# Performance work log

Hardware: AMD Instinct MI355X
Metric: run time of the kernel (lower is better)

The kernel has to match this reference:

```python
import jax, jax.numpy as jnp
import numpy as np

# geomloss SamplesLoss('sinkhorn', p=2, debias=True, reach=0.3, blur=0.01) constants
P = 2
BLUR = 0.01
REACH = 0.3
RHO = REACH ** P            # unbalanced KL strength rho = reach^p = 0.09
SCALING = 0.5               # geomloss default epsilon-scaling factor
DIAMETER = 1.0              # static diameter estimate (jit-friendly schedule)


def _eps_list():
    # geomloss epsilon_schedule(p, diameter, blur, scaling)
    eps = [DIAMETER ** P]
    eps += list(np.exp(np.arange(P * np.log(DIAMETER), P * np.log(BLUR), P * np.log(SCALING))))
    eps.append(BLUR ** P)
    return [float(e) for e in eps]


def _cost(x, y):
    # geomloss p=2 cost: |x - y|^2 / 2, shape [N, M]
    x2 = jnp.sum(x * x, axis=-1)[:, None]
    y2 = jnp.sum(y * y, axis=-1)[None, :]
    return 0.5 * (x2 + y2 - 2.0 * jnp.matmul(x, y.T))


def _softmin(eps, C, h):
    # h: log-weights (+ potential/eps), shape [M]; returns shape [N]
    return -eps * jax.nn.logsumexp(h[None, :] - C / eps, axis=1)


def _sinkhorn_divergence(x, y):
    N, M = x.shape[0], y.shape[0]
    a_log = jnp.full((N,), -np.log(N), dtype=x.dtype)   # uniform weights
    b_log = jnp.full((M,), -np.log(M), dtype=y.dtype)

    C_xy = _cost(x, y)
    C_yx = C_xy.T
    C_xx = _cost(x, x)
    C_yy = _cost(y, y)

    sg = jax.lax.stop_gradient
    Cxy_d, Cyx_d, Cxx_d, Cyy_d = sg(C_xy), sg(C_yx), sg(C_xx), sg(C_yy)

    eps_list = _eps_list()
    damp = lambda eps: 1.0 / (1.0 + eps / RHO)  # unbalanced dampening

    # init at largest blur (geomloss sinkhorn_loop)
    eps0 = eps_list[0]
    d0 = damp(eps0)
    g_ab = d0 * _softmin(eps0, Cyx_d, a_log)
    f_ba = d0 * _softmin(eps0, Cxy_d, b_log)
    f_aa = d0 * _softmin(eps0, Cxx_d, a_log)
    g_bb = d0 * _softmin(eps0, Cyy_d, b_log)

    # symmetric Sinkhorn updates with epsilon annealing (no grad, as in geomloss)
    for eps in eps_list:
        d = damp(eps)
        ft_ba = d * _softmin(eps, Cxy_d, b_log + g_ab / eps)
        gt_ab = d * _softmin(eps, Cyx_d, a_log + f_ba / eps)
        f_ba, g_ab = 0.5 * (f_ba + ft_ba), 0.5 * (g_ab + gt_ab)
        ft_aa = d * _softmin(eps, Cxx_d, a_log + f_aa / eps)
        gt_bb = d * _softmin(eps, Cyy_d, b_log + g_bb / eps)
        f_aa, g_bb = 0.5 * (f_aa + ft_aa), 0.5 * (g_bb + gt_bb)

    # last extrapolation at final blur, differentiable w.r.t. the cost
    eps = eps_list[-1]
    d = damp(eps)
    f_ba, g_ab = (d * _softmin(eps, C_xy, b_log + sg(g_ab) / eps),
                  d * _softmin(eps, C_yx, a_log + sg(f_ba) / eps))
    f_aa = d * _softmin(eps, C_xx, a_log + sg(f_aa) / eps)
    g_bb = d * _softmin(eps, C_yy, b_log + sg(g_bb) / eps)

    # unbalanced debiased Sinkhorn cost (geomloss sinkhorn_cost + UnbalancedWeight)
    a = jnp.exp(a_log)
    b = jnp.exp(b_log)
    w = RHO + eps / 2.0
    loss = w * (jnp.dot(a, jnp.exp(-f_aa / RHO) - jnp.exp(-f_ba / RHO))
                + jnp.dot(b, jnp.exp(-g_bb / RHO) - jnp.exp(-g_ab / RHO)))
    return loss


def setup_inputs() -> dict:
    key = jax.random.key(0)
    k1, k2, k3 = jax.random.split(key, 3)
    B, H, W = 512, 128, 128
    unnormed = jax.random.uniform(k1, (B, 1, H, W), dtype=jnp.float32)
    nd = jax.random.uniform(k2, (B, 1, H, W), dtype=jnp.float32)
    gt = jax.random.uniform(k3, (B, 1, H, W), dtype=jnp.float32)
    # normalized density maps sum to 1 per sample (as in DM-Count)
    nd = nd / jnp.sum(nd, axis=(1, 2, 3), keepdims=True)
    gt = gt / jnp.sum(gt, axis=(1, 2, 3), keepdims=True)
    return {"unnormed_density": unnormed, "normed_density": nd, "gt": gt}


def reference(unnormed_density, normed_density, gt):
    x = normed_density.reshape(normed_density.shape[0], -1)  # [B, HW]
    y = gt.reshape(gt.shape[0], -1)                          # [B, HW]
    loss = _sinkhorn_divergence(x, y)
    wd = 0
    ot_obj_values = jnp.zeros((1,), dtype=jnp.float32)
    return (loss, wd, ot_obj_values)
```

## Files before the change

### kernel.cpp

```cpp
#include <hip/hip_runtime.h>
#include <math.h>

#define HW 16384
#define NPTS 1024
#define LOG_N 6.2383246250395075
#define RHO_C 0.09
#define SCALE_F 16384.0f
#define INV_SCALE2 3.725290298461914e-09
#define NTILES 36

typedef _Float16 f16x8 __attribute__((ext_vector_type(8)));
typedef float f32x4 __attribute__((ext_vector_type(4)));

typedef __attribute__((address_space(1))) const void gvoid_t;
typedef __attribute__((address_space(3))) void svoid_t;

__device__ __forceinline__ void tri_map(int tt, int& ti, int& tj) {
  int a = 0, r = tt;
  while (r >= 8 - a) { r -= 8 - a; ++a; }
  ti = a; tj = a + r;
}

__global__ __launch_bounds__(256)
void convert_split_k(const float* __restrict__ nd, const float* __restrict__ gt,
                     _Float16* __restrict__ hi_t, _Float16* __restrict__ lo_t) {
  const int wt = blockIdx.x * 4 + (threadIdx.x >> 6);
  const int lane = threadIdx.x & 63;
  const int k64 = wt >> 6;
  const int rb = (wt & 63) << 4;
  const int g = lane & 7;
#pragma unroll
  for (int p = 0; p < 2; ++p) {
    const int row = rb + p * 8 + (lane >> 3);
    const float* __restrict__ src =
        (row < 512 ? nd + (size_t)row * HW : gt + (size_t)(row - 512) * HW) +
        k64 * 64 + g * 8;
    const float4 v0 = *(const float4*)(src);
    const float4 v1 = *(const float4*)(src + 4);
    const float x[8] = {v0.x, v0.y, v0.z, v0.w, v1.x, v1.y, v1.z, v1.w};
    f16x8 h, l;
#pragma unroll
    for (int j = 0; j < 8; ++j) {
      const float xs = x[j] * SCALE_F;
      const _Float16 hh = (_Float16)xs;
      h[j] = hh;
      l[j] = (_Float16)(xs - (float)hh);
    }
    const size_t o = ((size_t)k64 * 1024 + row) * 64 + (size_t)((g ^ (row & 7)) * 8);
    *(f16x8*)(hi_t + o) = h;
    *(f16x8*)(lo_t + o) = l;
  }
}

__global__ __launch_bounds__(512, 2)
void gemm_mfma_k(const _Float16* __restrict__ hi_t, const _Float16* __restrict__ lo_t,
                 float* __restrict__ part, int ns) {
  extern __shared__ _Float16 lds[];

  const int nwg = NTILES * ns;
  const int b = blockIdx.x;
  const int k8 = b & 7, i8 = b >> 3;
  const int q8 = nwg >> 3, r8 = nwg & 7;
  const int start = (k8 < r8) ? k8 * (q8 + 1) : r8 * (q8 + 1) + (k8 - r8) * q8;
  const int lin = start + i8;
  const int c = lin / NTILES, tt = lin - c * NTILES;

  int ti, tj;
  tri_map(tt, ti, tj);
  const bool dtile = (ti == tj);
  const int q = 256 / ns, rm = 256 - q * ns;
  const int kt0 = c * q + (c < rm ? c : rm);
  const int nkt = q + (c < rm ? 1 : 0);
  const int t = threadIdx.x;
  const int lane = t & 63, w = t >> 6;
  const int pr = (w >> 1) & 1, pc = w & 1;
  const int h = w >> 2;
  const int rlow = lane & 15, g0 = lane >> 4;
  const int sw = rlow & 7;
  const int boff = dtile ? 0 : 16384;

  f32x4 acc[4][4];
#pragma unroll
  for (int m = 0; m < 4; ++m)
#pragma unroll
    for (int n = 0; n < 4; ++n) acc[m][n] = (f32x4){0.f, 0.f, 0.f, 0.f};

#define STAGE(BUF, KT)                                                          \
  {                                                                             \
    const size_t tb_ = (size_t)(KT) * 65536;                                    \
    const size_t ga_ = tb_ + (size_t)ti * 8192 + w * 1024 + lane * 8;           \
    _Float16* lb_ = lds + (BUF) * 32768 + w * 1024;                             \
    __builtin_amdgcn_global_load_lds((gvoid_t*)(hi_t + ga_), (svoid_t*)(lb_), 16, 0, 0);               \
    __builtin_amdgcn_global_load_lds((gvoid_t*)(hi_t + ga_ + 512), (svoid_t*)(lb_ + 512), 16, 0, 0);   \
    __builtin_amdgcn_global_load_lds((gvoid_t*)(lo_t + ga_), (svoid_t*)(lb_ + 8192), 16, 0, 0);        \
    __builtin_amdgcn_global_load_lds((gvoid_t*)(lo_t + ga_ + 512), (svoid_t*)(lb_ + 8704), 16, 0, 0);  \
    if (!dtile) {                                                               \
      const size_t gb_ = tb_ + (size_t)tj * 8192 + w * 1024 + lane * 8;         \
      __builtin_amdgcn_global_load_lds((gvoid_t*)(hi_t + gb_), (svoid_t*)(lb_ + 16384), 16, 0, 0);     \
      __builtin_amdgcn_global_load_lds((gvoid_t*)(hi_t + gb_ + 512), (svoid_t*)(lb_ + 16896), 16, 0, 0);\
      __builtin_amdgcn_global_load_lds((gvoid_t*)(lo_t + gb_), (svoid_t*)(lb_ + 24576), 16, 0, 0);     \
      __builtin_amdgcn_global_load_lds((gvoid_t*)(lo_t + gb_ + 512), (svoid_t*)(lb_ + 25088), 16, 0, 0);\
    }                                                                           \
  }

  STAGE(0, kt0);
  __syncthreads();

  int cur = 0;
  for (int ks = 0; ks < nkt; ++ks) {
    if (ks + 1 < nkt) STAGE(cur ^ 1, kt0 + ks + 1);
    __builtin_amdgcn_sched_barrier(0);

    const _Float16* __restrict__ bb = lds + cur * 32768;
    const int pe = ((h * 4 + g0) ^ sw) * 8;
    f16x8 ah[4], al[4], bh[4], bl[4];
#pragma unroll
    for (int m = 0; m < 4; ++m) {
      const int ra = pr * 64 + m * 16 + rlow;
      ah[m] = *(const f16x8*)(bb + ra * 64 + pe);
      al[m] = *(const f16x8*)(bb + 8192 + ra * 64 + pe);
      const int rb = pc * 64 + m * 16 + rlow;
      bh[m] = *(const f16x8*)(bb + boff + rb * 64 + pe);
      bl[m] = *(const f16x8*)(bb + boff + 8192 + rb * 64 + pe);
    }

    __builtin_amdgcn_s_setprio(1);
#pragma unroll
    for (int m = 0; m < 4; ++m)
#pragma unroll
      for (int n = 0; n < 4; ++n) {
        acc[m][n] = __builtin_amdgcn_mfma_f32_16x16x32_f16(ah[m], bh[n], acc[m][n], 0, 0, 0);
        acc[m][n] = __builtin_amdgcn_mfma_f32_16x16x32_f16(al[m], bh[n], acc[m][n], 0, 0, 0);
        acc[m][n] = __builtin_amdgcn_mfma_f32_16x16x32_f16(ah[m], bl[n], acc[m][n], 0, 0, 0);
      }
    __builtin_amdgcn_s_setprio(0);
    __syncthreads();
    cur ^= 1;
  }

  float* red = (float*)lds;
  if (h == 1) {
    float* wb = red + (w & 3) * 4096;
#pragma unroll
    for (int m = 0; m < 4; ++m)
#pragma unroll
      for (int n = 0; n < 4; ++n)
        *(f32x4*)(wb + (m * 4 + n) * 256 + lane * 4) = acc[m][n];
  }
  __syncthreads();
  if (h == 0) {
    float* wb = red + w * 4096;
    float* __restrict__ dst = part + ((size_t)c * NTILES + tt) * 16384;
    const int clb = pc * 64 + rlow;
    const int rlb = pr * 64 + g0 * 4;
#pragma unroll
    for (int m = 0; m < 4; ++m)
#pragma unroll
      for (int n = 0; n < 4; ++n) {
        const f32x4 o = *(const f32x4*)(wb + (m * 4 + n) * 256 + lane * 4);
        const f32x4 s = acc[m][n] + o;
#pragma unroll
        for (int p = 0; p < 4; ++p)
          dst[(rlb + m * 16 + p) * 128 + clb + n * 16] = s[p];
      }
  }
#undef STAGE
}

__global__ __launch_bounds__(256)
void reduce_tiles_k(const float* __restrict__ part, float* __restrict__ G,
                    float* __restrict__ diag, int nsplit) {
  __shared__ float sl[8][129];
  const int blk = blockIdx.x;
  const int tt = blk >> 4, s = blk & 15;
  int ti, tj;
  tri_map(tt, ti, tj);
  const int t = threadIdx.x;
  const int base_in = tt * 16384 + s * 1024;

  float vals[4];
#pragma unroll
  for (int j = 0; j < 4; ++j) {
    const int idx = j * 256 + t;
    double a = 0.0;
    for (int c = 0; c < nsplit; ++c)
      a += (double)part[(size_t)c * (NTILES * 16384) + base_in + idx];
    vals[j] = (float)(a * INV_SCALE2);
  }
#pragma unroll
  for (int j = 0; j < 4; ++j) {
    const int idx = j * 256 + t;
    const int r = idx >> 7, cl = idx & 127;
    const int R = ti * 128 + s * 8 + r, C = tj * 128 + cl;
    G[(size_t)R * NPTS + C] = vals[j];
    if (R == C) diag[R] = vals[j];
    sl[r][cl] = vals[j];
  }
  if (ti == tj) return;
  __syncthreads();
#pragma unroll
  for (int j = 0; j < 4; ++j) {
    const int idx = j * 256 + t;
    const int r = idx & 7, cl = idx >> 3;
    G[(size_t)(tj * 128 + cl) * NPTS + ti * 128 + s * 8 + r] = sl[r][cl];
  }
}

__global__ __launch_bounds__(256)
void sinkhorn_phase_k(const float* __restrict__ G, const float* __restrict__ diag,
                      const double* __restrict__ src, double* __restrict__ dst,
                      double eps, double inv_eps, double damp, int use_pot,
                      int do_avg) {
  const int w = threadIdx.x >> 6, lane = threadIdx.x & 63;
  const int id = blockIdx.x * 4 + w;
  const int which = id >> 9, r = id & 511;
  int row_pt, col_base, pot_idx;
  if (which == 0)      { row_pt = r;       col_base = 512; pot_idx = 1; }
  else if (which == 1) { row_pt = 512 + r; col_base = 0;   pot_idx = 0; }
  else if (which == 2) { row_pt = r;       col_base = 0;   pot_idx = 2; }
  else                 { row_pt = 512 + r; col_base = 512; pot_idx = 3; }

  const double dr = (double)diag[row_pt];
  const double* __restrict__ pot = src + pot_idx * 512;
  const float* __restrict__ Grow = G + (size_t)row_pt * NPTS + col_base;
  const float* __restrict__ dcol = diag + col_base;

  double arg[8];
  double m = -1.0e300;
#pragma unroll
  for (int u = 0; u < 8; ++u) {
    const int j = lane + u * 64;
    const double C = 0.5 * (dr + (double)dcol[j]) - (double)Grow[j];
    const double p = use_pot ? pot[j] : 0.0;
    const double a = (p - C) * inv_eps - LOG_N;
    arg[u] = a;
    m = fmax(m, a);
  }
#pragma unroll
  for (int off = 32; off > 0; off >>= 1) m = fmax(m, __shfl_xor(m, off));
  double s = 0.0;
#pragma unroll
  for (int u = 0; u < 8; ++u) s += exp(arg[u] - m);
#pragma unroll
  for (int off = 32; off > 0; off >>= 1) s += __shfl_xor(s, off);
  if (lane == 0) {
    const double lse = m + log(s);
    const double val = -eps * lse * damp;
    dst[which * 512 + r] = do_avg ? 0.5 * (src[which * 512 + r] + val) : val;
  }
}

__global__ __launch_bounds__(256)
void loss_k(const double* __restrict__ pot, float* __restrict__ out, int out_size,
            double w) {
  const int t = threadIdx.x;
  double s = 0.0;
  for (int i = t; i < 512; i += 256) {
    s += (exp(-pot[1024 + i] / RHO_C) - exp(-pot[i] / RHO_C)) +
         (exp(-pot[1536 + i] / RHO_C) - exp(-pot[512 + i] / RHO_C));
  }
#pragma unroll
  for (int off = 32; off > 0; off >>= 1) s += __shfl_xor(s, off);
  __shared__ double wsum[4];
  if ((t & 63) == 0) wsum[t >> 6] = s;
  __syncthreads();
  if (t == 0) {
    out[0] = (float)(w * (wsum[0] + wsum[1] + wsum[2] + wsum[3]) * (1.0 / 512.0));
    for (int i = 1; i < out_size; ++i) out[i] = 0.f;
  }
}

extern "C" void kernel_launch(void* const* d_in, const int* in_sizes, int n_in,
                              void* d_out, int out_size, void* d_ws, size_t ws_size,
                              hipStream_t stream) {
  const float* nd = (const float*)d_in[1];
  const float* gt = (const float*)d_in[2];
  float* out = (float*)d_out;
  char* ws = (char*)d_ws;

  const size_t GM = (size_t)NPTS * NPTS;
  const size_t P16 = (size_t)NPTS * HW * 2;
  int nsplit = 7;
  while (nsplit > 1 &&
         2 * P16 + (size_t)nsplit * NTILES * 16384 * 4 + GM * 4 + 65536 > ws_size)
    nsplit >>= 1;

  _Float16* hi_t = (_Float16*)ws;
  _Float16* lo_t = (_Float16*)(ws + P16);
  float* part = (float*)(ws + 2 * P16);
  const size_t partsz = (size_t)nsplit * NTILES * 16384 * 4;
  float* G = (float*)(ws + 2 * P16 + partsz);
  float* diag = (float*)(ws + 2 * P16 + partsz + GM * 4);
  double* pots = (double*)(ws + 2 * P16 + partsz + GM * 4 + 8192);

  hipFuncSetAttribute((const void*)gemm_mfma_k,
                      hipFuncAttributeMaxDynamicSharedMemorySize, 131072);

  convert_split_k<<<4096, 256, 0, stream>>>(nd, gt, hi_t, lo_t);
  gemm_mfma_k<<<NTILES * nsplit, 512, 131072, stream>>>(hi_t, lo_t, part, nsplit);
  reduce_tiles_k<<<576, 256, 0, stream>>>(part, G, diag, nsplit);

  const double eps_list[9] = {1.0, 1.0, 0.25, 0.0625, 0.015625,
                              0.00390625, 0.0009765625, 0.000244140625, 1e-4};
  double* p0 = pots;
  double* p1 = pots + 2048;
  {
    const double eps = 1.0, d = 1.0 / (1.0 + eps / RHO_C);
    sinkhorn_phase_k<<<512, 256, 0, stream>>>(G, diag, p1, p0, eps, 1.0 / eps, d, 0, 0);
  }
  double* src = p0;
  double* dst = p1;
  for (int k = 0; k < 9; ++k) {
    const double eps = eps_list[k], d = 1.0 / (1.0 + eps / RHO_C);
    sinkhorn_phase_k<<<512, 256, 0, stream>>>(G, diag, src, dst, eps, 1.0 / eps, d, 1, 1);
    double* tmp = src; src = dst; dst = tmp;
  }
  {
    const double eps = 1e-4, d = 1.0 / (1.0 + eps / RHO_C);
    sinkhorn_phase_k<<<512, 256, 0, stream>>>(G, diag, src, dst, eps, 1.0 / eps, d, 1, 0);
    double* tmp = src; src = dst; dst = tmp;
  }
  loss_k<<<1, 256, 0, stream>>>(src, out, out_size, RHO_C + 1e-4 * 0.5);
}
```

Baseline: 139.1 us.

## Fuse Sinkhorn iterations and loss into one persistent kernel with grid barriers

Replaces the eleven per-phase Sinkhorn launches and the separate loss launch with a single persistent kernel of 256 blocks. Blocks synchronise between phases through an atomic counter barrier, and each wave keeps its cost-matrix entries in registers across all phases. This removes launch overhead and the repeated reloads of G and diag. In exchange it relies on all 256 blocks being co-resident for the spin barrier, and it adds atomic polling latency at every phase.

Result: slower. 208.4 us (+49.8%).

```diff
diff --git a/kernel.cpp b/kernel.cpp
--- a/kernel.cpp
+++ b/kernel.cpp
@@ -8,6 +8,7 @@
 #define SCALE_F 16384.0f
 #define INV_SCALE2 3.725290298461914e-09
 #define NTILES 36
+#define SINK_BLOCKS 256
 
 typedef _Float16 f16x8 __attribute__((ext_vector_type(8)));
 typedef float f32x4 __attribute__((ext_vector_type(4)));
@@ -206,67 +207,111 @@
   }
 }
 
+__device__ __forceinline__ double pot_ld(double* p) {
+  return __hip_atomic_load(p, __ATOMIC_RELAXED, __HIP_MEMORY_SCOPE_AGENT);
+}
+__device__ __forceinline__ void pot_st(double* p, double v) {
+  __hip_atomic_store(p, v, __ATOMIC_RELAXED, __HIP_MEMORY_SCOPE_AGENT);
+}
+
 __global__ __launch_bounds__(256)
-void sinkhorn_phase_k(const float* __restrict__ G, const float* __restrict__ diag,
-                      const double* __restrict__ src, double* __restrict__ dst,
-                      double eps, double inv_eps, double damp, int use_pot,
-                      int do_avg) {
+void sinkhorn_fused_k(const float* __restrict__ G, const float* __restrict__ diag,
+                      double* pots, unsigned* cnt, float* __restrict__ out,
+                      int out_size) {
   const int w = threadIdx.x >> 6, lane = threadIdx.x & 63;
-  const int id = blockIdx.x * 4 + w;
-  const int which = id >> 9, r = id & 511;
-  int row_pt, col_base, pot_idx;
-  if (which == 0)      { row_pt = r;       col_base = 512; pot_idx = 1; }
-  else if (which == 1) { row_pt = 512 + r; col_base = 0;   pot_idx = 0; }
-  else if (which == 2) { row_pt = r;       col_base = 0;   pot_idx = 2; }
-  else                 { row_pt = 512 + r; col_base = 512; pot_idx = 3; }
-
-  const double dr = (double)diag[row_pt];
-  const double* __restrict__ pot = src + pot_idx * 512;
-  const float* __restrict__ Grow = G + (size_t)row_pt * NPTS + col_base;
-  const float* __restrict__ dcol = diag + col_base;
-
-  double arg[8];
-  double m = -1.0e300;
-#pragma unroll
-  for (int u = 0; u < 8; ++u) {
-    const int j = lane + u * 64;
-    const double C = 0.5 * (dr + (double)dcol[j]) - (double)Grow[j];
-    const double p = use_pot ? pot[j] : 0.0;
-    const double a = (p - C) * inv_eps - LOG_N;
-    arg[u] = a;
-    m = fmax(m, a);
-  }
-#pragma unroll
-  for (int off = 32; off > 0; off >>= 1) m = fmax(m, __shfl_xor(m, off));
-  double s = 0.0;
-#pragma unroll
-  for (int u = 0; u < 8; ++u) s += exp(arg[u] - m);
-#pragma unroll
-  for (int off = 32; off > 0; off >>= 1) s += __shfl_xor(s, off);
-  if (lane == 0) {
-    const double lse = m + log(s);
-    const double val = -eps * lse * damp;
-    dst[which * 512 + r] = do_avg ? 0.5 * (src[which * 512 + r] + val) : val;
-  }
-}
-
-__global__ __launch_bounds__(256)
-void loss_k(const double* __restrict__ pot, float* __restrict__ out, int out_size,
-            double w) {
-  const int t = threadIdx.x;
-  double s = 0.0;
-  for (int i = t; i < 512; i += 256) {
-    s += (exp(-pot[1024 + i] / RHO_C) - exp(-pot[i] / RHO_C)) +
-         (exp(-pot[1536 + i] / RHO_C) - exp(-pot[512 + i] / RHO_C));
-  }
-#pragma unroll
-  for (int off = 32; off > 0; off >>= 1) s += __shfl_xor(s, off);
-  __shared__ double wsum[4];
-  if ((t & 63) == 0) wsum[t >> 6] = s;
-  __syncthreads();
-  if (t == 0) {
-    out[0] = (float)(w * (wsum[0] + wsum[1] + wsum[2] + wsum[3]) * (1.0 / 512.0));
-    for (int i = 1; i < out_size; ++i) out[i] = 0.f;
+  int which[2], rr[2], pot_idx[2];
+  double Creg[2][8];
+#pragma unroll
+  for (int s = 0; s < 2; ++s) {
+    const int id = blockIdx.x * 8 + w * 2 + s;
+    which[s] = id >> 9;
+    rr[s] = id & 511;
+    int row_pt, col_base;
+    if (which[s] == 0)      { row_pt = rr[s];       col_base = 512; pot_idx[s] = 1; }
+    else if (which[s] == 1) { row_pt = 512 + rr[s]; col_base = 0;   pot_idx[s] = 0; }
+    else if (which[s] == 2) { row_pt = rr[s];       col_base = 0;   pot_idx[s] = 2; }
+    else                    { row_pt = 512 + rr[s]; col_base = 512; pot_idx[s] = 3; }
+    const double dr = (double)diag[row_pt];
+    const float* __restrict__ Grow = G + (size_t)row_pt * NPTS + col_base;
+    const float* __restrict__ dcol = diag + col_base;
+#pragma unroll
+    for (int u = 0; u < 8; ++u) {
+      const int j = lane + u * 64;
+      Creg[s][u] = 0.5 * (dr + (double)dcol[j]) - (double)Grow[j];
+    }
+  }
+
+  double* buf0 = pots;
+  double* buf1 = pots + 2048;
+  const double eps_tab[11] = {1.0, 1.0, 1.0, 0.25, 0.0625, 0.015625,
+                              0.00390625, 0.0009765625, 0.000244140625, 1e-4, 1e-4};
+#pragma unroll
+  for (int p = 0; p < 11; ++p) {
+    const double eps = eps_tab[p];
+    const double inv_eps = 1.0 / eps;
+    const double damp = 1.0 / (1.0 + eps / RHO_C);
+    const int use_pot = (p > 0);
+    const int do_avg = (p >= 1 && p <= 9);
+    double* sp = (p & 1) ? buf0 : buf1;
+    double* dp = (p & 1) ? buf1 : buf0;
+#pragma unroll
+    for (int s = 0; s < 2; ++s) {
+      double* pot = sp + pot_idx[s] * 512;
+      double arg[8];
+      double m = -1.0e300;
+#pragma unroll
+      for (int u = 0; u < 8; ++u) {
+        const double pv = use_pot ? pot_ld(pot + lane + u * 64) : 0.0;
+        const double a = (pv - Creg[s][u]) * inv_eps - LOG_N;
+        arg[u] = a;
+        m = fmax(m, a);
+      }
+#pragma unroll
+      for (int off = 32; off > 0; off >>= 1) m = fmax(m, __shfl_xor(m, off));
+      double sm = 0.0;
+#pragma unroll
+      for (int u = 0; u < 8; ++u) sm += exp(arg[u] - m);
+#pragma unroll
+      for (int off = 32; off > 0; off >>= 1) sm += __shfl_xor(sm, off);
+      if (lane == 0) {
+        const double val = -eps * (m + log(sm)) * damp;
+        const int di = which[s] * 512 + rr[s];
+        const double fin = do_avg ? 0.5 * (pot_ld(sp + di) + val) : val;
+        pot_st(dp + di, fin);
+      }
+    }
+    asm volatile("s_waitcnt vmcnt(0)" ::: "memory");
+    __syncthreads();
+    if (threadIdx.x == 0) {
+      __hip_atomic_fetch_add(cnt, 1u, __ATOMIC_RELAXED, __HIP_MEMORY_SCOPE_AGENT);
+      const unsigned target = (unsigned)(SINK_BLOCKS * (p + 1));
+      int spins = 0;
+      while (__hip_atomic_load(cnt, __ATOMIC_RELAXED, __HIP_MEMORY_SCOPE_AGENT) < target &&
+             spins < (1 << 26)) {
+        __builtin_amdgcn_s_sleep(2);
+        ++spins;
+      }
+    }
+    __syncthreads();
+  }
+
+  if (blockIdx.x == 0) {
+    const int t = threadIdx.x;
+    double s = 0.0;
+    for (int i = t; i < 512; i += 256) {
+      s += (exp(-pot_ld(buf0 + 1024 + i) / RHO_C) - exp(-pot_ld(buf0 + i) / RHO_C)) +
+           (exp(-pot_ld(buf0 + 1536 + i) / RHO_C) - exp(-pot_ld(buf0 + 512 + i) / RHO_C));
+    }
+#pragma unroll
+    for (int off = 32; off > 0; off >>= 1) s += __shfl_xor(s, off);
+    __shared__ double wsum[4];
+    if ((t & 63) == 0) wsum[t >> 6] = s;
+    __syncthreads();
+    if (t == 0) {
+      const double tot = wsum[0] + wsum[1] + wsum[2] + wsum[3];
+      out[0] = (float)((RHO_C + 1e-4 * 0.5) * tot * (1.0 / 512.0));
+      for (int i = 1; i < out_size; ++i) out[i] = 0.f;
+    }
   }
 }
 
@@ -282,7 +327,7 @@
   const size_t P16 = (size_t)NPTS * HW * 2;
   int nsplit = 7;
   while (nsplit > 1 &&
-         2 * P16 + (size_t)nsplit * NTILES * 16384 * 4 + GM * 4 + 65536 > ws_size)
+         2 * P16 + (size_t)nsplit * NTILES * 16384 * 4 + GM * 4 + 131072 > ws_size)
     nsplit >>= 1;
 
   _Float16* hi_t = (_Float16*)ws;
@@ -292,33 +337,14 @@
   float* G = (float*)(ws + 2 * P16 + partsz);
   float* diag = (float*)(ws + 2 * P16 + partsz + GM * 4);
   double* pots = (double*)(ws + 2 * P16 + partsz + GM * 4 + 8192);
+  unsigned* cnt = (unsigned*)(ws + 2 * P16 + partsz + GM * 4 + 8192 + 65536);
 
   hipFuncSetAttribute((const void*)gemm_mfma_k,
                       hipFuncAttributeMaxDynamicSharedMemorySize, 131072);
 
+  hipMemsetAsync(cnt, 0, 64, stream);
   convert_split_k<<<4096, 256, 0, stream>>>(nd, gt, hi_t, lo_t);
   gemm_mfma_k<<<NTILES * nsplit, 512, 131072, stream>>>(hi_t, lo_t, part, nsplit);
   reduce_tiles_k<<<576, 256, 0, stream>>>(part, G, diag, nsplit);
-
-  const double eps_list[9] = {1.0, 1.0, 0.25, 0.0625, 0.015625,
-                              0.00390625, 0.0009765625, 0.000244140625, 1e-4};
-  double* p0 = pots;
-  double* p1 = pots + 2048;
-  {
-    const double eps = 1.0, d = 1.0 / (1.0 + eps / RHO_C);
-    sinkhorn_phase_k<<<512, 256, 0, stream>>>(G, diag, p1, p0, eps, 1.0 / eps, d, 0, 0);
-  }
-  double* src = p0;
-  double* dst = p1;
-  for (int k = 0; k < 9; ++k) {
-    const double eps = eps_list[k], d = 1.0 / (1.0 + eps / RHO_C);
-    sinkhorn_phase_k<<<512, 256, 0, stream>>>(G, diag, src, dst, eps, 1.0 / eps, d, 1, 1);
-    double* tmp = src; src = dst; dst = tmp;
-  }
-  {
-    const double eps = 1e-4, d = 1.0 / (1.0 + eps / RHO_C);
-    sinkhorn_phase_k<<<512, 256, 0, stream>>>(G, diag, src, dst, eps, 1.0 / eps, d, 1, 0);
-    double* tmp = src; src = dst; dst = tmp;
-  }
-  loss_k<<<1, 256, 0, stream>>>(src, out, out_size, RHO_C + 1e-4 * 0.5);
-}
+  sinkhorn_fused_k<<<SINK_BLOCKS, 256, 0, stream>>>(G, diag, pots, cnt, out, out_size);
+}
```
